# Kernel optimization log

Hardware: AMD Instinct MI355X
Metric: run time of the kernel (lower is better)

The kernel has to match this reference:

```python
import jax, jax.numpy as jnp
import numpy as np

EMBED_DIM = 1024
ATTN_DIM = 128
B, S = 4, 2048


def setup_inputs() -> dict:
    key = jax.random.key(0)
    k1, k2, k3, k4 = jax.random.split(key, 4)
    embedded = jax.random.normal(k1, (B, S, EMBED_DIM), dtype=jnp.float32)
    # torch nn.Linear weights are [out_features, in_features]
    scale = 1.0 / np.sqrt(EMBED_DIM)
    Wk = jax.random.uniform(k2, (ATTN_DIM, EMBED_DIM), dtype=jnp.float32, minval=-scale, maxval=scale)
    Wq = jax.random.uniform(k3, (ATTN_DIM, EMBED_DIM), dtype=jnp.float32, minval=-scale, maxval=scale)
    Wv = jax.random.uniform(k4, (ATTN_DIM, EMBED_DIM), dtype=jnp.float32, minval=-scale, maxval=scale)
    return {"embedded": embedded, "Wk": Wk, "Wq": Wq, "Wv": Wv}


def reference(embedded, Wk, Wq, Wv):
    # projections (no bias): x @ W.T
    k = jnp.einsum('bse,ae->bsa', embedded, Wk)  # [B,S,A]
    q = jnp.einsum('bse,ae->bsa', embedded, Wq)
    v = jnp.einsum('bse,ae->bsa', embedded, Wv)
    ad = k.shape[-1]
    scores = jnp.einsum('bqa,bka->bqk', q, k) / jnp.sqrt(jnp.float32(ad))  # [B,S,S]
    causal = jnp.tril(jnp.ones((scores.shape[1], scores.shape[1]), dtype=bool))
    scores = jnp.where(causal, scores, -jnp.inf)
    probs = jax.nn.softmax(scores, axis=-1)
    out = jnp.einsum('bqk,bka->bqa', probs, v)
    return jnp.round(out, 4)
```

## Files before the change

kernel.cpp:

```cpp
#include <hip/hip_runtime.h>
#include <hip/hip_bf16.h>
#include <math.h>

#define B 4
#define S 2048
#define E 1024
#define A 128

typedef __attribute__((ext_vector_type(8))) short short8;
typedef __attribute__((ext_vector_type(4))) float floatx4;

static __device__ __forceinline__ short f2bf(float f) {
  union { float f; unsigned u; } c;
  c.f = f;
  unsigned r = (c.u + 0x7fffu + ((c.u >> 16) & 1u)) >> 16;
  return (short)r;
}
static __device__ __forceinline__ unsigned f2bf2(float x, float y) {
  __hip_bfloat162 h = __float22bfloat162_rn(float2{x, y});
  union { __hip_bfloat162 h; unsigned u; } c;
  c.h = h;
  return c.u;
}

#define PJ 72
#define CN 130
__global__ __launch_bounds__(256) void proj_gemm(
    const float* __restrict__ X,
    const float* __restrict__ Wq,
    const float* __restrict__ Wk,
    const float* __restrict__ Wv,
    short* __restrict__ Qbf,
    short* __restrict__ Kbf,
    short* __restrict__ Vt) {
  __shared__ __align__(16) char smem[27648];
  short* As = (short*)smem;
  short* Bs = (short*)(smem + 9216);
  short* Cs = (short*)smem;

  const int m0 = blockIdx.x * 64;
  const int which = blockIdx.y;
  const float* Wp = (which == 0) ? Wq : (which == 1) ? Wk : Wv;

  const int tid = threadIdx.x;
  const int wave = tid >> 6;
  const int lane = tid & 63;
  const int mh = wave & 1;
  const int nh = wave >> 1;
  const int l16 = lane & 15;
  const int quad = lane >> 4;

  int arow[4], ac4[4], brow[8], bc4[8];
#pragma unroll
  for (int i = 0; i < 4; ++i) {
    const int fa = tid + i * 256;
    arow[i] = fa >> 4; ac4[i] = fa & 15;
  }
#pragma unroll
  for (int i = 0; i < 8; ++i) {
    const int fb = tid + i * 256;
    brow[i] = fb >> 4; bc4[i] = fb & 15;
  }

  floatx4 acc[2][4] = {};
  float4 aplf[4];
  float4 wplf[8];

#pragma unroll
  for (int i = 0; i < 4; ++i)
    aplf[i] = *(const float4*)&X[(size_t)(m0 + arow[i]) * E + ac4[i] * 4];
#pragma unroll
  for (int i = 0; i < 8; ++i)
    wplf[i] = *(const float4*)&Wp[(size_t)brow[i] * E + bc4[i] * 4];

  for (int k0 = 0; k0 < E; k0 += 64) {
    __syncthreads();
#pragma unroll
    for (int i = 0; i < 4; ++i) {
      uint2 p; p.x = f2bf2(aplf[i].x, aplf[i].y); p.y = f2bf2(aplf[i].z, aplf[i].w);
      *(uint2*)&As[arow[i] * PJ + ac4[i] * 4] = p;
    }
#pragma unroll
    for (int i = 0; i < 8; ++i) {
      uint2 p; p.x = f2bf2(wplf[i].x, wplf[i].y); p.y = f2bf2(wplf[i].z, wplf[i].w);
      *(uint2*)&Bs[brow[i] * PJ + bc4[i] * 4] = p;
    }
    __syncthreads();

    if (k0 + 64 < E) {
#pragma unroll
      for (int i = 0; i < 4; ++i)
        aplf[i] = *(const float4*)&X[(size_t)(m0 + arow[i]) * E + (k0 + 64) + ac4[i] * 4];
#pragma unroll
      for (int i = 0; i < 8; ++i)
        wplf[i] = *(const float4*)&Wp[(size_t)brow[i] * E + (k0 + 64) + bc4[i] * 4];
    }

    short8 afr[2][2], bfr[4][2];
#pragma unroll
    for (int ms = 0; ms < 2; ++ms)
#pragma unroll
      for (int ks = 0; ks < 2; ++ks)
        afr[ms][ks] = *(const short8*)&As[(mh * 32 + ms * 16 + l16) * PJ + ks * 32 + quad * 8];
#pragma unroll
    for (int nt = 0; nt < 4; ++nt)
#pragma unroll
      for (int ks = 0; ks < 2; ++ks)
        bfr[nt][ks] = *(const short8*)&Bs[(nh * 64 + nt * 16 + l16) * PJ + ks * 32 + quad * 8];

#pragma unroll
    for (int ms = 0; ms < 2; ++ms)
#pragma unroll
      for (int nt = 0; nt < 4; ++nt)
#pragma unroll
        for (int ks = 0; ks < 2; ++ks)
          acc[ms][nt] = __builtin_amdgcn_mfma_f32_16x16x32_bf16(
              afr[ms][ks], bfr[nt][ks], acc[ms][nt], 0, 0, 0);
  }

  const float qscale = 0.08838834764831845f;
  if (which == 2) {
#pragma unroll
    for (int ms = 0; ms < 2; ++ms) {
#pragma unroll
      for (int nt = 0; nt < 4; ++nt) {
        const int n = nh * 64 + nt * 16 + l16;
        const int mbase = m0 + mh * 32 + ms * 16 + quad * 4;
        const int b = mbase >> 11, s = mbase & (S - 1);
        short4 p;
        p.x = f2bf(acc[ms][nt][0]); p.y = f2bf(acc[ms][nt][1]);
        p.z = f2bf(acc[ms][nt][2]); p.w = f2bf(acc[ms][nt][3]);
        *(short4*)&Vt[((size_t)b * A + n) * S + s] = p;
      }
    }
  } else {
    __syncthreads();
    const float sc = (which == 0) ? qscale : 1.0f;
#pragma unroll
    for (int ms = 0; ms < 2; ++ms)
#pragma unroll
      for (int nt = 0; nt < 4; ++nt)
#pragma unroll
        for (int r = 0; r < 4; ++r)
          Cs[(mh * 32 + ms * 16 + quad * 4 + r) * CN + nh * 64 + nt * 16 + l16] =
              f2bf(acc[ms][nt][r] * sc);
    __syncthreads();
    short* Outp = (which == 0) ? Qbf : Kbf;
#pragma unroll
    for (int i = 0; i < 4; ++i) {
      const int f = tid + i * 256;
      const int row = f >> 4, c8 = f & 15;
      *(short8*)&Outp[(size_t)(m0 + row) * A + c8 * 8] =
          *(const short8*)&Cs[row * CN + c8 * 8];
    }
  }
}

#define LK2 132
#define LV2 132
__global__ __launch_bounds__(256) void attn_fused(
    const short* __restrict__ Qbf,
    const short* __restrict__ Kbf,
    const short* __restrict__ Vt,
    float* __restrict__ Out) {
  __shared__ short Ks[128 * LK2];
  __shared__ short Vs[64 * LV2];
  __shared__ short Ps[4][16 * LV2];

  const int idx = (int)blockIdx.x;
  const int r2 = idx >> 1;
  const int ah = idx & 1;
  const int iq = 31 - (r2 >> 2);
  const int b = r2 & 3;
  const int q0 = iq << 6;
  const int nk = q0 + 64;
  const int ntiles = (nk + 127) >> 7;

  const int tid = threadIdx.x;
  const int wave = tid >> 6;
  const int lane = tid & 63;
  const int l16 = lane & 15;
  const int quad = lane >> 4;

  int krow[8], kc8[8], vrow[4], vc8[4];
#pragma unroll
  for (int i = 0; i < 8; ++i) {
    const int f = tid + i * 256;
    krow[i] = f >> 4; kc8[i] = f & 15;
  }
#pragma unroll
  for (int i = 0; i < 4; ++i) {
    const int f = tid + i * 256;
    vrow[i] = f >> 4; vc8[i] = f & 15;
  }

  short8 qfr[4];
  {
    const size_t qrow = (size_t)(b * S + q0 + wave * 16 + l16);
#pragma unroll
    for (int ks = 0; ks < 4; ++ks)
      qfr[ks] = *(const short8*)&Qbf[qrow * A + ks * 32 + quad * 8];
  }

  float l_acc[4] = {0.f, 0.f, 0.f, 0.f};
  floatx4 oacc[4] = {};

  const int myrow = q0 + wave * 16 + quad * 4;
  const short* Kbase = Kbf + (size_t)b * S * A;
  const short* Vbase = Vt + ((size_t)b * A + ah * 64) * S;

  short8 kplf[8], vplf[4];
#pragma unroll
  for (int i = 0; i < 8; ++i)
    kplf[i] = *(const short8*)&Kbase[(size_t)krow[i] * A + kc8[i] * 8];
#pragma unroll
  for (int i = 0; i < 4; ++i)
    vplf[i] = *(const short8*)&Vbase[(size_t)vrow[i] * S + vc8[i] * 8];

  for (int t = 0; t < ntiles; ++t) {
    const int j0 = t * 128;
    __syncthreads();
#pragma unroll
    for (int i = 0; i < 8; ++i)
      *(short8*)&Ks[krow[i] * LK2 + kc8[i] * 8] = kplf[i];
#pragma unroll
    for (int i = 0; i < 4; ++i)
      *(short8*)&Vs[vrow[i] * LV2 + vc8[i] * 8] = vplf[i];
    __syncthreads();

    if (t + 1 < ntiles) {
      const int jn = j0 + 128;
#pragma unroll
      for (int i = 0; i < 8; ++i)
        kplf[i] = *(const short8*)&Kbase[(size_t)(jn + krow[i]) * A + kc8[i] * 8];
#pragma unroll
      for (int i = 0; i < 4; ++i)
        vplf[i] = *(const short8*)&Vbase[(size_t)vrow[i] * S + jn + vc8[i] * 8];
    }

    floatx4 sc[8];
#pragma unroll
    for (int nt = 0; nt < 8; ++nt) {
      floatx4 c = {};
#pragma unroll
      for (int ks = 0; ks < 4; ++ks) {
        const short8 bfr = *(const short8*)&Ks[(nt * 16 + l16) * LK2 + ks * 32 + quad * 8];
        c = __builtin_amdgcn_mfma_f32_16x16x32_bf16(qfr[ks], bfr, c, 0, 0, 0);
      }
      sc[nt] = c;
    }

#pragma unroll
    for (int nt = 0; nt < 8; ++nt) {
      const int key = j0 + nt * 16 + l16;
#pragma unroll
      for (int r = 0; r < 4; ++r) {
        const float p = (key > myrow + r) ? 0.f : __expf(sc[nt][r]);
        sc[nt][r] = p;
        l_acc[r] += p;
      }
    }

#pragma unroll
    for (int nt = 0; nt < 8; ++nt)
#pragma unroll
      for (int r = 0; r < 4; ++r)
        Ps[wave][(quad * 4 + r) * LV2 + nt * 16 + l16] = f2bf(sc[nt][r]);

    short8 pfr[4];
#pragma unroll
    for (int ks = 0; ks < 4; ++ks)
      pfr[ks] = *(const short8*)&Ps[wave][l16 * LV2 + ks * 32 + quad * 8];

#pragma unroll
    for (int nt = 0; nt < 4; ++nt) {
#pragma unroll
      for (int ks = 0; ks < 4; ++ks) {
        const short8 vfr = *(const short8*)&Vs[(nt * 16 + l16) * LV2 + ks * 32 + quad * 8];
        oacc[nt] = __builtin_amdgcn_mfma_f32_16x16x32_bf16(pfr[ks], vfr, oacc[nt], 0, 0, 0);
      }
    }
  }

#pragma unroll
  for (int r = 0; r < 4; ++r) {
    float l = l_acc[r];
    l += __shfl_xor(l, 1);
    l += __shfl_xor(l, 2);
    l += __shfl_xor(l, 4);
    l += __shfl_xor(l, 8);
    l_acc[r] = 1.f / l;
  }
#pragma unroll
  for (int nt = 0; nt < 4; ++nt) {
    const int col = ah * 64 + nt * 16 + l16;
#pragma unroll
    for (int r = 0; r < 4; ++r) {
      const size_t row = (size_t)(b * S + myrow + r);
      Out[row * A + col] = oacc[nt][r] * l_acc[r];
    }
  }
}

extern "C" void kernel_launch(void* const* d_in, const int* in_sizes, int n_in,
                              void* d_out, int out_size, void* d_ws, size_t ws_size,
                              hipStream_t stream) {
  const float* X  = (const float*)d_in[0];
  const float* Wk = (const float*)d_in[1];
  const float* Wq = (const float*)d_in[2];
  const float* Wv = (const float*)d_in[3];
  float* Out = (float*)d_out;

  const size_t qkv_elems = (size_t)B * S * A;
  short* Qbf = (short*)d_ws;
  short* Kbf = Qbf + qkv_elems;
  short* Vt  = Kbf + qkv_elems;

  dim3 pgrid(B * S / 64, 3);
  proj_gemm<<<pgrid, 256, 0, stream>>>(X, Wq, Wk, Wv, Qbf, Kbf, Vt);
  attn_fused<<<(B * S / 64) * 2, 256, 0, stream>>>(Qbf, Kbf, Vt, Out);
}
```

Before: 134.7 us.

## Compute transposed scores so P feeds PV MFMA directly from registers

Swaps operand order in the QK^T MFMA so each lane holds scores for one query row and four consecutive keys. That layout matches the B operand of a 16x16x16 bf16 MFMA, so the probabilities are packed to bf16 in registers and fed straight into a transposed PV accumulation. This removes the per-wave shared-memory P buffer and its write/read round trip. It also simplifies the row-sum reduction and lets the output be written with float4 stores. In exchange the PV product uses the smaller K=16 MFMA (more instructions) and narrower 8-byte V reads from LDS.

```diff
diff --git a/kernel.cpp b/kernel.cpp
--- a/kernel.cpp
+++ b/kernel.cpp
@@ -7,8 +7,26 @@
 #define E 1024
 #define A 128
 
+typedef __attribute__((ext_vector_type(4))) short shortx4;
 typedef __attribute__((ext_vector_type(8))) short short8;
 typedef __attribute__((ext_vector_type(4))) float floatx4;
+
+#if defined(__has_builtin)
+#if __has_builtin(__builtin_amdgcn_mfma_f32_16x16x16bf16_1k)
+#define HAVE_MFMA16 1
+#endif
+#endif
+#ifdef HAVE_MFMA16
+#define MFMA16(Av, Bv, Cv) __builtin_amdgcn_mfma_f32_16x16x16bf16_1k((Av), (Bv), (Cv), 0, 0, 0)
+#else
+static __device__ __forceinline__ floatx4 mfma16_asm(shortx4 a, shortx4 b, floatx4 c) {
+  floatx4 d;
+  asm("v_mfma_f32_16x16x16_bf16 %0, %1, %2, %3"
+      : "=v"(d) : "v"(a), "v"(b), "v"(c));
+  return d;
+}
+#define MFMA16(Av, Bv, Cv) mfma16_asm((Av), (Bv), (Cv))
+#endif
 
 static __device__ __forceinline__ short f2bf(float f) {
   union { float f; unsigned u; } c;
@@ -165,7 +183,6 @@
     float* __restrict__ Out) {
   __shared__ short Ks[128 * LK2];
   __shared__ short Vs[64 * LV2];
-  __shared__ short Ps[4][16 * LV2];
 
   const int idx = (int)blockIdx.x;
   const int r2 = idx >> 1;
@@ -194,18 +211,18 @@
     vrow[i] = f >> 4; vc8[i] = f & 15;
   }
 
+  const int qrow = q0 + wave * 16 + l16;
   short8 qfr[4];
   {
-    const size_t qrow = (size_t)(b * S + q0 + wave * 16 + l16);
+    const size_t qr = (size_t)(b * S + qrow);
 #pragma unroll
     for (int ks = 0; ks < 4; ++ks)
-      qfr[ks] = *(const short8*)&Qbf[qrow * A + ks * 32 + quad * 8];
-  }
-
-  float l_acc[4] = {0.f, 0.f, 0.f, 0.f};
-  floatx4 oacc[4] = {};
-
-  const int myrow = q0 + wave * 16 + quad * 4;
+      qfr[ks] = *(const short8*)&Qbf[qr * A + ks * 32 + quad * 8];
+  }
+
+  float l_acc = 0.f;
+  floatx4 oaccT[4] = {};
+
   const short* Kbase = Kbf + (size_t)b * S * A;
   const short* Vbase = Vt + ((size_t)b * A + ah * 64) * S;
 
@@ -238,67 +255,46 @@
         vplf[i] = *(const short8*)&Vbase[(size_t)vrow[i] * S + jn + vc8[i] * 8];
     }
 
-    floatx4 sc[8];
 #pragma unroll
     for (int nt = 0; nt < 8; ++nt) {
-      floatx4 c = {};
+      floatx4 st = {};
 #pragma unroll
       for (int ks = 0; ks < 4; ++ks) {
-        const short8 bfr = *(const short8*)&Ks[(nt * 16 + l16) * LK2 + ks * 32 + quad * 8];
-        c = __builtin_amdgcn_mfma_f32_16x16x32_bf16(qfr[ks], bfr, c, 0, 0, 0);
+        const short8 kfr = *(const short8*)&Ks[(nt * 16 + l16) * LK2 + ks * 32 + quad * 8];
+        st = __builtin_amdgcn_mfma_f32_16x16x32_bf16(kfr, qfr[ks], st, 0, 0, 0);
       }
-      sc[nt] = c;
-    }
-
-#pragma unroll
-    for (int nt = 0; nt < 8; ++nt) {
-      const int key = j0 + nt * 16 + l16;
+      float pr[4];
 #pragma unroll
       for (int r = 0; r < 4; ++r) {
-        const float p = (key > myrow + r) ? 0.f : __expf(sc[nt][r]);
-        sc[nt][r] = p;
-        l_acc[r] += p;
+        const int key = j0 + nt * 16 + quad * 4 + r;
+        const float p = (key > qrow) ? 0.f : __expf(st[r]);
+        pr[r] = p;
+        l_acc += p;
       }
-    }
-
-#pragma unroll
-    for (int nt = 0; nt < 8; ++nt)
-#pragma unroll
-      for (int r = 0; r < 4; ++r)
-        Ps[wave][(quad * 4 + r) * LV2 + nt * 16 + l16] = f2bf(sc[nt][r]);
-
-    short8 pfr[4];
-#pragma unroll
-    for (int ks = 0; ks < 4; ++ks)
-      pfr[ks] = *(const short8*)&Ps[wave][l16 * LV2 + ks * 32 + quad * 8];
-
-#pragma unroll
-    for (int nt = 0; nt < 4; ++nt) {
-#pragma unroll
-      for (int ks = 0; ks < 4; ++ks) {
-        const short8 vfr = *(const short8*)&Vs[(nt * 16 + l16) * LV2 + ks * 32 + quad * 8];
-        oacc[nt] = __builtin_amdgcn_mfma_f32_16x16x32_bf16(pfr[ks], vfr, oacc[nt], 0, 0, 0);
+      union { uint2 u; shortx4 s; } pk;
+      pk.u.x = f2bf2(pr[0], pr[1]);
+      pk.u.y = f2bf2(pr[2], pr[3]);
+      const shortx4 pfrB = pk.s;
+
+#pragma unroll
+      for (int at = 0; at < 4; ++at) {
+        const shortx4 vfr = *(const shortx4*)&Vs[(at * 16 + l16) * LV2 + nt * 16 + quad * 4];
+        oaccT[at] = MFMA16(vfr, pfrB, oaccT[at]);
       }
     }
   }
 
-#pragma unroll
-  for (int r = 0; r < 4; ++r) {
-    float l = l_acc[r];
-    l += __shfl_xor(l, 1);
-    l += __shfl_xor(l, 2);
-    l += __shfl_xor(l, 4);
-    l += __shfl_xor(l, 8);
-    l_acc[r] = 1.f / l;
-  }
-#pragma unroll
-  for (int nt = 0; nt < 4; ++nt) {
-    const int col = ah * 64 + nt * 16 + l16;
-#pragma unroll
-    for (int r = 0; r < 4; ++r) {
-      const size_t row = (size_t)(b * S + myrow + r);
-      Out[row * A + col] = oacc[nt][r] * l_acc[r];
-    }
+  l_acc += __shfl_xor(l_acc, 16);
+  l_acc += __shfl_xor(l_acc, 32);
+  const float inv = 1.f / l_acc;
+
+  const size_t row = (size_t)(b * S + qrow);
+#pragma unroll
+  for (int at = 0; at < 4; ++at) {
+    float4 v;
+    v.x = oaccT[at][0] * inv; v.y = oaccT[at][1] * inv;
+    v.z = oaccT[at][2] * inv; v.w = oaccT[at][3] * inv;
+    *(float4*)&Out[row * A + ah * 64 + at * 16 + quad * 4] = v;
   }
 }
 
```

Result: no change. 132.4 us (-1.7%).
